# Optimization experiments

Hardware: AMD Instinct MI355X
Metric: run time of the kernel (lower is better)

## Reference

```python
import jax, jax.numpy as jnp
import numpy as np

N = 262144
H = 256
R = 32


def setup_inputs() -> dict:
    key = jax.random.key(0)
    ks = jax.random.split(key, 16)
    s = 1.0 / np.sqrt(H)
    return {
        "x": jax.random.normal(ks[0], (N, 1), jnp.float32),
        "t": jax.random.uniform(ks[1], (N, 1), jnp.float32),
        "start_w": jax.random.normal(ks[2], (H, 2), jnp.float32) * 0.5,
        "start_b": jax.random.normal(ks[3], (H,), jnp.float32) * 0.1,
        "end_w": jax.random.normal(ks[4], (1, H), jnp.float32) * s,
        "end_b": jax.random.normal(ks[5], (1,), jnp.float32) * 0.1,
        "col_0": jax.random.normal(ks[6], (H, R), jnp.float32) * s,
        "col_1": jax.random.normal(ks[7], (H, R), jnp.float32) * s,
        "col_2": jax.random.normal(ks[8], (H, R), jnp.float32) * s,
        "row_0": jax.random.normal(ks[9], (H, R), jnp.float32) * s,
        "row_1": jax.random.normal(ks[10], (H, R), jnp.float32) * s,
        "row_2": jax.random.normal(ks[11], (H, R), jnp.float32) * s,
        "alpha_0": jax.random.normal(ks[12], (R,), jnp.float32),
        "alpha_1": jax.random.normal(ks[13], (R,), jnp.float32),
        "alpha_2": jax.random.normal(ks[14], (R,), jnp.float32),
    }


def reference(x, t, start_w, start_b, end_w, end_b,
              col_0, col_1, col_2, row_0, row_1, row_2,
              alpha_0, alpha_1, alpha_2):
    # inputs: [N,2] -> start Linear -> tanh
    inp = jnp.concatenate([x, t], axis=1)
    h = jnp.tanh(inp @ start_w.T + start_b)  # [N, H]
    # three low-rank blocks: h @ (col * diag(alpha)) @ row.T, then tanh.
    # col_basis @ diag(alpha) == col_basis * alpha[None, :] (column scaling)
    for col, row, alpha in ((col_0, row_0, alpha_0),
                            (col_1, row_1, alpha_1),
                            (col_2, row_2, alpha_2)):
        h = jnp.tanh((h @ (col * alpha)) @ row.T)  # [N,H]->[N,R]->[N,H]
    return h @ end_w.T + end_b  # [N, 1]
```

## Files before the change

kernel.cpp:

```cpp
#include <hip/hip_runtime.h>


typedef _Float16 half8_t __attribute__((ext_vector_type(8)));
typedef _Float16 half4_t __attribute__((ext_vector_type(4)));
typedef __fp16   fp16x2  __attribute__((ext_vector_type(2)));
typedef float    float4_t __attribute__((ext_vector_type(4)));

#define TANH_SCALE 2.885390081777927f
#define MFMA32 __builtin_amdgcn_mfma_f32_16x16x32_f16

namespace {

struct alignas(16) Smem {
  half8_t ctf[3 * 8 * 2 * 64];
  half8_t rwf[3 * 16 * 64];
  float w0[256], w1[256], bb[256];
  float ew[256];
  float rsC[3 * 32];
};

__device__ __forceinline__ half4_t pack4(float4_t v) {
  union { fp16x2 f2[2]; half4_t h4; } u;
  u.f2[0] = __builtin_amdgcn_cvt_pkrtz(v.x, v.y);
  u.f2[1] = __builtin_amdgcn_cvt_pkrtz(v.z, v.w);
  return u.h4;
}

__device__ __forceinline__ half8_t combine8(half4_t lo, half4_t hi) {
  union { half4_t h4[2]; half8_t h8; } u;
  u.h4[0] = lo; u.h4[1] = hi;
  return u.h8;
}

__device__ __forceinline__ float inv_pre(float y) {
  return __builtin_amdgcn_rcpf(__builtin_amdgcn_exp2f(y) + 1.0f);
}

__device__ __forceinline__ half4_t inv4(float4_t v) {
  float4_t r;
  r.x = inv_pre(v.x); r.y = inv_pre(v.y);
  r.z = inv_pre(v.z); r.w = inv_pre(v.w);
  return pack4(r);
}

__global__ __launch_bounds__(1024)
__attribute__((amdgpu_waves_per_eu(4, 4)))
void pinn_fused(
    const float* __restrict__ xg, const float* __restrict__ tg,
    const float* __restrict__ sw, const float* __restrict__ sb,
    const float* __restrict__ ewp, const float* __restrict__ ebp,
    const float* __restrict__ c0, const float* __restrict__ c1,
    const float* __restrict__ c2, const float* __restrict__ r0,
    const float* __restrict__ r1, const float* __restrict__ r2,
    const float* __restrict__ a0, const float* __restrict__ a1,
    const float* __restrict__ a2, float* __restrict__ out, int n)
{
  __shared__ Smem sm;
  const int tid = threadIdx.x;

  for (int e = tid; e < 3 * 8 * 2 * 64; e += 1024) {
    const int lane_ = e & 63;
    const int sel   = (e >> 6) & 1;
    const int T_    = (e >> 7) & 7;
    const int k_    = e >> 10;
    const int m_ = lane_ & 15, q_ = lane_ >> 4;
    const float* ck = (k_ == 0) ? c0 : (k_ == 1) ? c1 : c2;
    const float* ak = (k_ == 0) ? a0 : (k_ == 1) ? a1 : a2;
    const int rp_ = 8 * (m_ >> 2) + (m_ & 3) + 4 * sel;
    const float av = ak[rp_] * -2.0f;
    const int h0 = 32 * T_ + 8 * q_;
    half8_t v;
#pragma unroll
    for (int j = 0; j < 8; ++j)
      v[j] = (_Float16)(ck[(h0 + j) * 32 + rp_] * av);
    sm.ctf[e] = v;
  }
  for (int e = tid; e < 3 * 16 * 64; e += 1024) {
    const int lane_ = e & 63;
    const int tp    = (e >> 6) & 15;
    const int k_    = e >> 10;
    const int m_ = lane_ & 15, q_ = lane_ >> 4;
    const float* rk = (k_ == 0) ? r0 : (k_ == 1) ? r1 : r2;
    const int hrow = 32 * (tp >> 1) + 8 * (m_ >> 2) + 4 * (tp & 1) + (m_ & 3);
    half8_t v;
#pragma unroll
    for (int j = 0; j < 8; ++j)
      v[j] = (_Float16)(rk[hrow * 32 + 8 * q_ + j] * TANH_SCALE);
    sm.rwf[e] = v;
  }
  if (tid < 256) {
    sm.w0[tid] = sw[2 * tid] * TANH_SCALE;
    sm.w1[tid] = sw[2 * tid + 1] * TANH_SCALE;
    sm.bb[tid] = sb[tid] * TANH_SCALE;
    const int tp = tid >> 4, ii = tid & 15;
    const int hph = 32 * (tp >> 1) + 8 * (ii >> 2) + 4 * (tp & 1) + (ii & 3);
    sm.ew[tid] = ewp[hph] * -2.0f;
  }
  __syncthreads();

  if (tid < 96) {
    const int k_ = tid >> 5, r = tid & 31;
    const int sel = r >> 4, mm = r & 15;
    float s = 0.0f;
    for (int T = 0; T < 8; ++T)
      for (int qq = 0; qq < 4; ++qq) {
        const half8_t v = sm.ctf[((k_ * 8 + T) * 2 + sel) * 64 + 16 * qq + mm];
        float ps = 0.0f;
#pragma unroll
        for (int j = 0; j < 8; ++j) ps += (float)v[j];
        s += ps;
      }
    sm.rsC[k_ * 32 + r] = -0.5f * s;
  }
  __syncthreads();

  const int wave = tid >> 6;
  const int lane = tid & 63;
  const int m = lane & 15;
  const int q = lane >> 4;
  const int wo = 4 * q;
  const int wo8 = 8 * q;
  const float ebv = ebp[0];
  const int tiles = n >> 4;

  float ewsum = 0.0f;
  for (int t = 0; t < 16; ++t) {
    const float4_t e4 = *(const float4_t*)&sm.ew[t * 16 + wo];
    ewsum += e4.x + e4.y + e4.z + e4.w;
  }
  ewsum *= -0.5f;

  const float4_t z4 = {0.f, 0.f, 0.f, 0.f};

#pragma unroll 1
  for (int g = (blockIdx.x * 16 + wave) * 4; g < tiles; g += 16384) {
    float xm[4], tm[4];
#pragma unroll
    for (int s = 0; s < 4; ++s) {
      xm[s] = xg[(g + s) * 16 + m];
      tm[s] = tg[(g + s) * 16 + m];
    }

    const float4_t rs00 = *(const float4_t*)&sm.rsC[wo];
    const float4_t rs01 = *(const float4_t*)&sm.rsC[16 + wo];
    float4_t acc[4][2];
#pragma unroll
    for (int s = 0; s < 4; ++s) { acc[s][0] = rs00; acc[s][1] = rs01; }
    const half8_t* cp0 = &sm.ctf[lane];
#pragma unroll 1
    for (int T = 0; T < 8; ++T) {
      const int cb = 32 * T + wo8;
      const float4_t w0a = *(const float4_t*)&sm.w0[cb];
      const float4_t w0b = *(const float4_t*)&sm.w0[cb + 4];
      const float4_t w1a = *(const float4_t*)&sm.w1[cb];
      const float4_t w1b = *(const float4_t*)&sm.w1[cb + 4];
      const float4_t ba  = *(const float4_t*)&sm.bb[cb];
      const float4_t bb2 = *(const float4_t*)&sm.bb[cb + 4];
      half8_t h[4];
#pragma unroll
      for (int s = 0; s < 4; ++s) {
        float4_t za, zb;
        za.x = fmaf(xm[s], w0a.x, fmaf(tm[s], w1a.x, ba.x));
        za.y = fmaf(xm[s], w0a.y, fmaf(tm[s], w1a.y, ba.y));
        za.z = fmaf(xm[s], w0a.z, fmaf(tm[s], w1a.z, ba.z));
        za.w = fmaf(xm[s], w0a.w, fmaf(tm[s], w1a.w, ba.w));
        zb.x = fmaf(xm[s], w0b.x, fmaf(tm[s], w1b.x, bb2.x));
        zb.y = fmaf(xm[s], w0b.y, fmaf(tm[s], w1b.y, bb2.y));
        zb.z = fmaf(xm[s], w0b.z, fmaf(tm[s], w1b.z, bb2.z));
        zb.w = fmaf(xm[s], w0b.w, fmaf(tm[s], w1b.w, bb2.w));
        h[s] = combine8(inv4(za), inv4(zb));
      }
      const half8_t cA = cp0[0], cB = cp0[64];
#pragma unroll
      for (int s = 0; s < 4; ++s) acc[s][0] = MFMA32(cA, h[s], acc[s][0], 0, 0, 0);
#pragma unroll
      for (int s = 0; s < 4; ++s) acc[s][1] = MFMA32(cB, h[s], acc[s][1], 0, 0, 0);
      cp0 += 128;
    }

#pragma unroll 1
    for (int k = 0; k < 2; ++k) {
      half8_t pf[4];
#pragma unroll
      for (int s = 0; s < 4; ++s)
        pf[s] = combine8(pack4(acc[s][0]), pack4(acc[s][1]));
      const float4_t rsA = *(const float4_t*)&sm.rsC[(k + 1) * 32 + wo];
      const float4_t rsB = *(const float4_t*)&sm.rsC[(k + 1) * 32 + 16 + wo];
      float4_t nn[4][2];
#pragma unroll
      for (int s = 0; s < 4; ++s) { nn[s][0] = rsA; nn[s][1] = rsB; }
      const half8_t* rp = &sm.rwf[k * 1024 + lane];
      const half8_t* cp = &sm.ctf[(k + 1) * 1024 + lane];
#pragma unroll 1
      for (int t2 = 0; t2 < 8; ++t2) {
        const half8_t rA = rp[0], rB = rp[64];
        const half8_t cA = cp[0], cB = cp[64];
        float4_t u0[4];
#pragma unroll
        for (int s = 0; s < 4; ++s) u0[s] = MFMA32(rA, pf[s], z4, 0, 0, 0);
        half4_t hl[4];
#pragma unroll
        for (int s = 0; s < 4; ++s) hl[s] = inv4(u0[s]);
        float4_t u1[4];
#pragma unroll
        for (int s = 0; s < 4; ++s) u1[s] = MFMA32(rB, pf[s], z4, 0, 0, 0);
        half8_t h[4];
#pragma unroll
        for (int s = 0; s < 4; ++s) h[s] = combine8(hl[s], inv4(u1[s]));
#pragma unroll
        for (int s = 0; s < 4; ++s) nn[s][0] = MFMA32(cA, h[s], nn[s][0], 0, 0, 0);
#pragma unroll
        for (int s = 0; s < 4; ++s) nn[s][1] = MFMA32(cB, h[s], nn[s][1], 0, 0, 0);
        rp += 128; cp += 128;
      }
#pragma unroll
      for (int s = 0; s < 4; ++s) { acc[s][0] = nn[s][0]; acc[s][1] = nn[s][1]; }
    }

    float ssum[4] = {ewsum, ewsum, ewsum, ewsum};
    {
      half8_t pf[4];
#pragma unroll
      for (int s = 0; s < 4; ++s)
        pf[s] = combine8(pack4(acc[s][0]), pack4(acc[s][1]));
      const half8_t* rp = &sm.rwf[2 * 1024 + lane];
#pragma unroll 1
      for (int tp = 0; tp < 16; ++tp) {
        const half8_t rA = rp[0];
        const float4_t ev = *(const float4_t*)&sm.ew[tp * 16 + wo];
        float4_t u[4];
#pragma unroll
        for (int s = 0; s < 4; ++s) u[s] = MFMA32(rA, pf[s], z4, 0, 0, 0);
#pragma unroll
        for (int s = 0; s < 4; ++s) {
          ssum[s] = fmaf(ev.x, inv_pre(u[s].x), ssum[s]);
          ssum[s] = fmaf(ev.y, inv_pre(u[s].y), ssum[s]);
          ssum[s] = fmaf(ev.z, inv_pre(u[s].z), ssum[s]);
          ssum[s] = fmaf(ev.w, inv_pre(u[s].w), ssum[s]);
        }
        rp += 64;
      }
    }

#pragma unroll
    for (int s = 0; s < 4; ++s) {
      ssum[s] += __shfl_xor(ssum[s], 16);
      ssum[s] += __shfl_xor(ssum[s], 32);
    }
    if (lane < 16) {
#pragma unroll
      for (int s = 0; s < 4; ++s) out[(g + s) * 16 + m] = ssum[s] + ebv;
    }
  }
}

}

extern "C" void kernel_launch(void* const* d_in, const int* in_sizes, int n_in,
                              void* d_out, int out_size, void* d_ws, size_t ws_size,
                              hipStream_t stream) {
  const float* xg  = (const float*)d_in[0];
  const float* tg  = (const float*)d_in[1];
  const float* sw  = (const float*)d_in[2];
  const float* sb  = (const float*)d_in[3];
  const float* ewp = (const float*)d_in[4];
  const float* ebp = (const float*)d_in[5];
  const float* c0  = (const float*)d_in[6];
  const float* c1  = (const float*)d_in[7];
  const float* c2  = (const float*)d_in[8];
  const float* r0  = (const float*)d_in[9];
  const float* r1  = (const float*)d_in[10];
  const float* r2  = (const float*)d_in[11];
  const float* a0  = (const float*)d_in[12];
  const float* a1  = (const float*)d_in[13];
  const float* a2  = (const float*)d_in[14];
  float* outp = (float*)d_out;

  const int n = in_sizes[0];

  pinn_fused<<<256, 1024, 0, stream>>>(xg, tg, sw, sb, ewp, ebp,
                                       c0, c1, c2, r0, r1, r2, a0, a1, a2,
                                       outp, n);
}
```

Baseline: 138.0 us.

## Software-pipeline LDS weight loads and prefetch x/t before shared-memory setup

```diff
diff --git a/kernel.cpp b/kernel.cpp
--- a/kernel.cpp
+++ b/kernel.cpp
@@ -57,6 +57,23 @@
 {
   __shared__ Smem sm;
   const int tid = threadIdx.x;
+  const int wave = tid >> 6;
+  const int lane = tid & 63;
+  const int m = lane & 15;
+  const int q = lane >> 4;
+  const int wo = 4 * q;
+  const int wo8 = 8 * q;
+  const int tiles = n >> 4;
+
+  const int g0 = (blockIdx.x * 16 + wave) * 4;
+  float xm[4], tm[4];
+  if (g0 < tiles) {
+#pragma unroll
+    for (int s = 0; s < 4; ++s) {
+      xm[s] = xg[(g0 + s) * 16 + m];
+      tm[s] = tg[(g0 + s) * 16 + m];
+    }
+  }
 
   for (int e = tid; e < 3 * 8 * 2 * 64; e += 1024) {
     const int lane_ = e & 63;
@@ -114,14 +131,7 @@
   }
   __syncthreads();
 
-  const int wave = tid >> 6;
-  const int lane = tid & 63;
-  const int m = lane & 15;
-  const int q = lane >> 4;
-  const int wo = 4 * q;
-  const int wo8 = 8 * q;
   const float ebv = ebp[0];
-  const int tiles = n >> 4;
 
   float ewsum = 0.0f;
   for (int t = 0; t < 16; ++t) {
@@ -133,29 +143,30 @@
   const float4_t z4 = {0.f, 0.f, 0.f, 0.f};
 
 #pragma unroll 1
-  for (int g = (blockIdx.x * 16 + wave) * 4; g < tiles; g += 16384) {
-    float xm[4], tm[4];
-#pragma unroll
-    for (int s = 0; s < 4; ++s) {
-      xm[s] = xg[(g + s) * 16 + m];
-      tm[s] = tg[(g + s) * 16 + m];
-    }
-
+  for (int g = g0; g < tiles; g += 16384) {
     const float4_t rs00 = *(const float4_t*)&sm.rsC[wo];
     const float4_t rs01 = *(const float4_t*)&sm.rsC[16 + wo];
     float4_t acc[4][2];
 #pragma unroll
     for (int s = 0; s < 4; ++s) { acc[s][0] = rs00; acc[s][1] = rs01; }
     const half8_t* cp0 = &sm.ctf[lane];
+    half8_t cA = cp0[0], cB = cp0[64];
+    float4_t w0a = *(const float4_t*)&sm.w0[wo8];
+    float4_t w0b = *(const float4_t*)&sm.w0[wo8 + 4];
+    float4_t w1a = *(const float4_t*)&sm.w1[wo8];
+    float4_t w1b = *(const float4_t*)&sm.w1[wo8 + 4];
+    float4_t ba  = *(const float4_t*)&sm.bb[wo8];
+    float4_t bb2 = *(const float4_t*)&sm.bb[wo8 + 4];
 #pragma unroll 1
     for (int T = 0; T < 8; ++T) {
-      const int cb = 32 * T + wo8;
-      const float4_t w0a = *(const float4_t*)&sm.w0[cb];
-      const float4_t w0b = *(const float4_t*)&sm.w0[cb + 4];
-      const float4_t w1a = *(const float4_t*)&sm.w1[cb];
-      const float4_t w1b = *(const float4_t*)&sm.w1[cb + 4];
-      const float4_t ba  = *(const float4_t*)&sm.bb[cb];
-      const float4_t bb2 = *(const float4_t*)&sm.bb[cb + 4];
+      const half8_t cAn = cp0[128], cBn = cp0[192];
+      const int cbn = 32 * T + 32 + wo8;
+      const float4_t w0an = *(const float4_t*)&sm.w0[cbn];
+      const float4_t w0bn = *(const float4_t*)&sm.w0[cbn + 4];
+      const float4_t w1an = *(const float4_t*)&sm.w1[cbn];
+      const float4_t w1bn = *(const float4_t*)&sm.w1[cbn + 4];
+      const float4_t ban  = *(const float4_t*)&sm.bb[cbn];
+      const float4_t bb2n = *(const float4_t*)&sm.bb[cbn + 4];
       half8_t h[4];
 #pragma unroll
       for (int s = 0; s < 4; ++s) {
@@ -170,11 +181,12 @@
         zb.w = fmaf(xm[s], w0b.w, fmaf(tm[s], w1b.w, bb2.w));
         h[s] = combine8(inv4(za), inv4(zb));
       }
-      const half8_t cA = cp0[0], cB = cp0[64];
 #pragma unroll
       for (int s = 0; s < 4; ++s) acc[s][0] = MFMA32(cA, h[s], acc[s][0], 0, 0, 0);
 #pragma unroll
       for (int s = 0; s < 4; ++s) acc[s][1] = MFMA32(cB, h[s], acc[s][1], 0, 0, 0);
+      cA = cAn; cB = cBn;
+      w0a = w0an; w0b = w0bn; w1a = w1an; w1b = w1bn; ba = ban; bb2 = bb2n;
       cp0 += 128;
     }
 
@@ -191,10 +203,12 @@
       for (int s = 0; s < 4; ++s) { nn[s][0] = rsA; nn[s][1] = rsB; }
       const half8_t* rp = &sm.rwf[k * 1024 + lane];
       const half8_t* cp = &sm.ctf[(k + 1) * 1024 + lane];
+      half8_t rA = rp[0], rB = rp[64];
+      half8_t cA = cp[0], cB = cp[64];
 #pragma unroll 1
       for (int t2 = 0; t2 < 8; ++t2) {
-        const half8_t rA = rp[0], rB = rp[64];
-        const half8_t cA = cp[0], cB = cp[64];
+        const half8_t rAn = rp[128], rBn = rp[192];
+        const half8_t cAn = cp[128], cBn = cp[192];
         float4_t u0[4];
 #pragma unroll
         for (int s = 0; s < 4; ++s) u0[s] = MFMA32(rA, pf[s], z4, 0, 0, 0);
@@ -211,6 +225,7 @@
         for (int s = 0; s < 4; ++s) nn[s][0] = MFMA32(cA, h[s], nn[s][0], 0, 0, 0);
 #pragma unroll
         for (int s = 0; s < 4; ++s) nn[s][1] = MFMA32(cB, h[s], nn[s][1], 0, 0, 0);
+        rA = rAn; rB = rBn; cA = cAn; cB = cBn;
         rp += 128; cp += 128;
       }
 #pragma unroll
@@ -224,10 +239,12 @@
       for (int s = 0; s < 4; ++s)
         pf[s] = combine8(pack4(acc[s][0]), pack4(acc[s][1]));
       const half8_t* rp = &sm.rwf[2 * 1024 + lane];
+      half8_t rA = rp[0];
+      float4_t ev = *(const float4_t*)&sm.ew[wo];
 #pragma unroll 1
       for (int tp = 0; tp < 16; ++tp) {
-        const half8_t rA = rp[0];
-        const float4_t ev = *(const float4_t*)&sm.ew[tp * 16 + wo];
+        const half8_t rAn = rp[64];
+        const float4_t evn = *(const float4_t*)&sm.ew[tp * 16 + 16 + wo];
         float4_t u[4];
 #pragma unroll
         for (int s = 0; s < 4; ++s) u[s] = MFMA32(rA, pf[s], z4, 0, 0, 0);
@@ -238,6 +255,7 @@
           ssum[s] = fmaf(ev.z, inv_pre(u[s].z), ssum[s]);
           ssum[s] = fmaf(ev.w, inv_pre(u[s].w), ssum[s]);
         }
+        rA = rAn; ev = evn;
         rp += 64;
       }
     }
@@ -250,6 +268,15 @@
     if (lane < 16) {
 #pragma unroll
       for (int s = 0; s < 4; ++s) out[(g + s) * 16 + m] = ssum[s] + ebv;
+    }
+
+    const int gn = g + 16384;
+    if (gn < tiles) {
+#pragma unroll
+      for (int s = 0; s < 4; ++s) {
+        xm[s] = xg[(gn + s) * 16 + m];
+        tm[s] = tg[(gn + s) * 16 + m];
+      }
     }
   }
 }
```

Result: slower. 145.2 us (+5.2%).

## Prefetch inputs before setup, stagger wave cohorts, and prioritize MFMA issue

Applied to the files above, without the earlier changes.

```diff
diff --git a/kernel.cpp b/kernel.cpp
--- a/kernel.cpp
+++ b/kernel.cpp
@@ -57,6 +57,23 @@
 {
   __shared__ Smem sm;
   const int tid = threadIdx.x;
+  const int wave = tid >> 6;
+  const int lane = tid & 63;
+  const int m = lane & 15;
+  const int q = lane >> 4;
+  const int wo = 4 * q;
+  const int wo8 = 8 * q;
+  const int tiles = n >> 4;
+
+  const int g0 = (blockIdx.x * 16 + wave) * 4;
+  float xm[4], tm[4];
+  if (g0 < tiles) {
+#pragma unroll
+    for (int s = 0; s < 4; ++s) {
+      xm[s] = xg[(g0 + s) * 16 + m];
+      tm[s] = tg[(g0 + s) * 16 + m];
+    }
+  }
 
   for (int e = tid; e < 3 * 8 * 2 * 64; e += 1024) {
     const int lane_ = e & 63;
@@ -114,14 +131,14 @@
   }
   __syncthreads();
 
-  const int wave = tid >> 6;
-  const int lane = tid & 63;
-  const int m = lane & 15;
-  const int q = lane >> 4;
-  const int wo = 4 * q;
-  const int wo8 = 8 * q;
+  {
+    const int cohort = wave >> 2;
+    if (cohort > 0) __builtin_amdgcn_s_sleep(7);
+    if (cohort > 1) __builtin_amdgcn_s_sleep(7);
+    if (cohort > 2) __builtin_amdgcn_s_sleep(7);
+  }
+
   const float ebv = ebp[0];
-  const int tiles = n >> 4;
 
   float ewsum = 0.0f;
   for (int t = 0; t < 16; ++t) {
@@ -133,14 +150,7 @@
   const float4_t z4 = {0.f, 0.f, 0.f, 0.f};
 
 #pragma unroll 1
-  for (int g = (blockIdx.x * 16 + wave) * 4; g < tiles; g += 16384) {
-    float xm[4], tm[4];
-#pragma unroll
-    for (int s = 0; s < 4; ++s) {
-      xm[s] = xg[(g + s) * 16 + m];
-      tm[s] = tg[(g + s) * 16 + m];
-    }
-
+  for (int g = g0; g < tiles; g += 16384) {
     const float4_t rs00 = *(const float4_t*)&sm.rsC[wo];
     const float4_t rs01 = *(const float4_t*)&sm.rsC[16 + wo];
     float4_t acc[4][2];
@@ -171,10 +181,12 @@
         h[s] = combine8(inv4(za), inv4(zb));
       }
       const half8_t cA = cp0[0], cB = cp0[64];
+      __builtin_amdgcn_s_setprio(1);
 #pragma unroll
       for (int s = 0; s < 4; ++s) acc[s][0] = MFMA32(cA, h[s], acc[s][0], 0, 0, 0);
 #pragma unroll
       for (int s = 0; s < 4; ++s) acc[s][1] = MFMA32(cB, h[s], acc[s][1], 0, 0, 0);
+      __builtin_amdgcn_s_setprio(0);
       cp0 += 128;
     }
 
@@ -196,21 +208,27 @@
         const half8_t rA = rp[0], rB = rp[64];
         const half8_t cA = cp[0], cB = cp[64];
         float4_t u0[4];
+        __builtin_amdgcn_s_setprio(1);
 #pragma unroll
         for (int s = 0; s < 4; ++s) u0[s] = MFMA32(rA, pf[s], z4, 0, 0, 0);
+        __builtin_amdgcn_s_setprio(0);
         half4_t hl[4];
 #pragma unroll
         for (int s = 0; s < 4; ++s) hl[s] = inv4(u0[s]);
         float4_t u1[4];
+        __builtin_amdgcn_s_setprio(1);
 #pragma unroll
         for (int s = 0; s < 4; ++s) u1[s] = MFMA32(rB, pf[s], z4, 0, 0, 0);
+        __builtin_amdgcn_s_setprio(0);
         half8_t h[4];
 #pragma unroll
         for (int s = 0; s < 4; ++s) h[s] = combine8(hl[s], inv4(u1[s]));
+        __builtin_amdgcn_s_setprio(1);
 #pragma unroll
         for (int s = 0; s < 4; ++s) nn[s][0] = MFMA32(cA, h[s], nn[s][0], 0, 0, 0);
 #pragma unroll
         for (int s = 0; s < 4; ++s) nn[s][1] = MFMA32(cB, h[s], nn[s][1], 0, 0, 0);
+        __builtin_amdgcn_s_setprio(0);
         rp += 128; cp += 128;
       }
 #pragma unroll
@@ -229,8 +247,10 @@
         const half8_t rA = rp[0];
         const float4_t ev = *(const float4_t*)&sm.ew[tp * 16 + wo];
         float4_t u[4];
+        __builtin_amdgcn_s_setprio(1);
 #pragma unroll
         for (int s = 0; s < 4; ++s) u[s] = MFMA32(rA, pf[s], z4, 0, 0, 0);
+        __builtin_amdgcn_s_setprio(0);
 #pragma unroll
         for (int s = 0; s < 4; ++s) {
           ssum[s] = fmaf(ev.x, inv_pre(u[s].x), ssum[s]);
@@ -250,6 +270,15 @@
     if (lane < 16) {
 #pragma unroll
       for (int s = 0; s < 4; ++s) out[(g + s) * 16 + m] = ssum[s] + ebv;
+    }
+
+    const int gn = g + 16384;
+    if (gn < tiles) {
+#pragma unroll
+      for (int s = 0; s < 4; ++s) {
+        xm[s] = xg[(gn + s) * 16 + m];
+        tm[s] = tg[(gn + s) * 16 + m];
+      }
     }
   }
 }
```

New measurement: 138.5 us. Within noise of the previous version (+0.4%).
